# Kernel tuning notes

Hardware: AMD Instinct MI355X
Metric: run time of the kernel (lower is better)

## Reference

```python
import jax, jax.numpy as jnp
import numpy as np
import math

B, L = 16, 4096
N = B * L            # total nodes; node 0 is the (masked) root
E = N - 1            # one parent edge per non-root node
D_IN, D_OUT, HEADS = 512, 256, 4
SLOPE = 0.2          # PyG GATConv default negative_slope
PRUNE_FRAC = 0.3


def gelu(x):
    return 0.5 * x * (1.0 + jnp.tanh(math.sqrt(2.0 / math.pi) * (x + 0.044715 * x ** 3)))


def remove_nodes_func(parent, remove):
    # parent[i] = parent node id of node i+1; remove[j] = 1 iff node j+1 removed.
    for _ in range(5):
        aug_rem = jnp.concatenate([jnp.zeros(1, jnp.int32), remove])
        aug_par = jnp.concatenate([jnp.zeros(1, jnp.int32), parent])
        pr = aug_rem[parent]                               # is my parent removed?
        parent = pr * aug_par[parent] + (1 - pr) * parent  # grandparent if so
    return parent


def remove_nodes_and_edges(edge_index, map_index):
    src, par = edge_index[0], edge_index[1]
    rem = jnp.zeros(N, jnp.int32).at[map_index].set(1)     # removal flag per node id (>=1)
    edge_mask = 1 - rem[src]                               # drop edges whose child node removed
    emr = rem[1:]                                          # == zeros(E).at[map_index-1].set(1)
    temp = remove_nodes_func(par, emr)
    ei_new = jnp.stack([src, temp]) * edge_mask[None, :]   # removed edges collapse to (0,0)
    node_mask_upd = jnp.concatenate([jnp.ones(1, jnp.float32), 1.0 - emr.astype(jnp.float32)])
    return ei_new, node_mask_upd


def gat_conv(xin, edge_index, gat_w, att_src, att_dst, gat_b):
    # PyG GATConv: concat=True, add_self_loops=True, eval mode (attention dropout off)
    h = (xin @ gat_w).reshape(N, HEADS, D_OUT)
    loop = jnp.arange(N, dtype=edge_index.dtype)
    src = jnp.concatenate([edge_index[0], loop])
    dst = jnp.concatenate([edge_index[1], loop])
    a_src = jnp.einsum('nhc,hc->nh', h, att_src)
    a_dst = jnp.einsum('nhc,hc->nh', h, att_dst)
    alpha = jax.nn.leaky_relu(a_src[src] + a_dst[dst], SLOPE)       # [Etot, H]
    m = jax.ops.segment_max(alpha, dst, num_segments=N)
    e = jnp.exp(alpha - m[dst])
    s = jax.ops.segment_sum(e, dst, num_segments=N)
    coef = e / (s[dst] + 1e-16)
    out = jax.ops.segment_sum(coef[:, :, None] * h[src], dst, num_segments=N)
    return out.reshape(N, HEADS * D_OUT) + gat_b


def setup_inputs():
    key = jax.random.key(0)
    ks = jax.random.split(key, 10)
    x = jax.random.normal(ks[0], (N, D_IN), jnp.float32)
    statement_rep = jax.random.normal(ks[1], (N, D_IN), jnp.float32)
    node_mask = (jax.random.uniform(ks[2], (B, L)) > 0.3).astype(jnp.float32)
    node_mask = node_mask.at[0, 0].set(0.0)  # root node never scored/pruned
    type_id = jax.random.randint(ks[3], (B, L), 0, 2, dtype=jnp.int32)
    child = jnp.arange(1, N, dtype=jnp.int32)
    parent = jnp.floor(jax.random.uniform(ks[4], (E,)) * child).astype(jnp.int32)  # parent < child
    edge_index = jnp.stack([child, parent])
    edge_index_ent = edge_index
    s = 0.02
    scorer_w = jax.random.normal(ks[5], (2 * D_IN, 1), jnp.float32) * s
    scorer_b = jnp.zeros((1,), jnp.float32)
    emb_w = jax.random.normal(ks[6], (2, D_OUT), jnp.float32) * s
    emb_b = jnp.zeros((D_OUT,), jnp.float32)
    gat_w = jax.random.normal(ks[7], (2 * D_IN + D_OUT, HEADS * D_OUT), jnp.float32) * s
    att_src = jax.random.normal(ks[8], (HEADS, D_OUT), jnp.float32) * s
    att_dst = jax.random.normal(ks[9], (HEADS, D_OUT), jnp.float32) * s
    gat_b = jnp.zeros((HEADS * D_OUT,), jnp.float32)
    return {"x": x, "edge_index": edge_index, "edge_index_ent": edge_index_ent,
            "statement_rep": statement_rep, "node_mask": node_mask, "type_id": type_id,
            "scorer_w": scorer_w, "scorer_b": scorer_b, "emb_w": emb_w, "emb_b": emb_b,
            "gat_w": gat_w, "att_src": att_src, "att_dst": att_dst, "gat_b": gat_b}


def reference(x, edge_index, edge_index_ent, statement_rep, node_mask, type_id,
              scorer_w, scorer_b, emb_w, emb_b, gat_w, att_src, att_dst, gat_b):
    del edge_index_ent  # threaded through the original but never used
    nm = node_mask.reshape(-1)
    tid = type_id.reshape(-1)
    one_hot = jax.nn.one_hot(tid, 2, dtype=jnp.float32)
    type_emb = gelu(one_hot @ emb_w + emb_b)
    # --- single GNN layer (num_layers=1), with top-k node pruning ---
    node_score = (jnp.concatenate([x, statement_rep], 1) @ scorer_w + scorer_b)[:, 0] * nm
    nnz = int(jnp.count_nonzero(node_score))  # eager; k is data-dependent in the original
    if int(nnz * PRUNE_FRAC) != 0:
        k = int(nnz * PRUNE_FRAC + 1)
        masked = jnp.where(node_score != 0, node_score, jnp.inf)
        _, map_index = jax.lax.top_k(-masked, k)  # k smallest nonzero scores -> node ids
        edge_index, upd = remove_nodes_and_edges(edge_index, map_index)
        nm = nm * upd
    xin = jnp.concatenate([x, statement_rep, type_emb], 1)
    out = gelu(gat_conv(xin, edge_index, gat_w, att_src, att_dst, gat_b))
    # feature dropout runs in eval as identity here (deterministic reference)
    return out, nm.reshape(B, L)
```

## Files before the change

### kernel.cpp

```cpp
#include <hip/hip_runtime.h>
#include <cstdint>
#include <cstddef>

#define N_NODES 65536
#define E_EDGES 65535
#define DIN     512
#define KDIM    1024
#define JDIM    1024
#define HEADS   4
#define DOUT    256

typedef short   short8  __attribute__((ext_vector_type(8)));
typedef float   floatx4 __attribute__((ext_vector_type(4)));

__device__ inline float bf2f(unsigned short u){
  union { unsigned int i; float f; } c; c.i = ((unsigned int)u) << 16; return c.f;
}
__device__ inline unsigned short f2bf(float f){
  union { float f; unsigned int i; } c; c.f = f;
  unsigned int r = c.i + 0x7FFFu + ((c.i >> 16) & 1u);
  return (unsigned short)(r >> 16);
}
__device__ inline unsigned int okey(float f){
  union { float f; unsigned int u; } c; c.f = f;
  return (c.u & 0x80000000u) ? ~c.u : (c.u | 0x80000000u);
}
__device__ inline float unokey(unsigned int k){
  union { unsigned int u; float f; } c;
  c.u = (k & 0x80000000u) ? (k ^ 0x80000000u) : ~k;
  return c.f;
}
__device__ inline float leaky(float x){ return x >= 0.f ? x : 0.2f * x; }
__device__ inline float gelu_f(float x){
  return 0.5f * x * (1.f + tanhf(0.7978845608028654f * (x + 0.044715f * x * x * x)));
}

__global__ void k_prep(const float* __restrict__ x, const float* __restrict__ sr,
                       const float* __restrict__ nmask, const float* __restrict__ sw,
                       const float* __restrict__ sb, unsigned short* __restrict__ xs,
                       float* __restrict__ score){
  int i = blockIdx.x, t = threadIdx.x;
  float4 v;
  if (t < 128) v = *(const float4*)(x  + (size_t)i*DIN + 4*t);
  else         v = *(const float4*)(sr + (size_t)i*DIN + 4*(t-128));
  const float4 w = *(const float4*)(sw + 4*t);
  double part = (double)v.x*(double)w.x + (double)v.y*(double)w.y
              + (double)v.z*(double)w.z + (double)v.w*(double)w.w;
  ushort4 o; o.x = f2bf(v.x); o.y = f2bf(v.y); o.z = f2bf(v.z); o.w = f2bf(v.w);
  *(ushort4*)(xs + (size_t)i*KDIM + 4*t) = o;
  for (int sdel = 32; sdel; sdel >>= 1) part += __shfl_down(part, sdel);
  __shared__ double red[4];
  if ((t & 63) == 0) red[t >> 6] = part;
  __syncthreads();
  if (t == 0){
    double s = red[0] + red[1] + red[2] + red[3] + (double)sb[0];
    score[i] = (float)s * nmask[i];
  }
}

__global__ void k_nnz(const float* __restrict__ score, int* scal){
  int i = blockIdx.x*256 + threadIdx.x;
  int nz = (score[i] != 0.f) ? 1 : 0;
  unsigned long long b = __ballot(nz);
  if ((threadIdx.x & 63) == 0) atomicAdd(&scal[0], (int)__popcll(b));
}

__global__ void k_makekey(const float* __restrict__ score, unsigned int* __restrict__ key){
  int i = blockIdx.x*256 + threadIdx.x;
  float v = score[i];
  if (v == 0.f) v = __builtin_inff();
  key[i] = okey(v);
}

__global__ void k_initsel(int* scal){
  int nnz = scal[0];
  double prod = (double)nnz * 0.3;
  scal[1] = ((int)prod != 0) ? 1 : 0;
  int k = (int)(prod + 1.0);
  scal[2] = k; scal[3] = 0; scal[4] = k;
}

__global__ void k_hist(const unsigned int* __restrict__ key, unsigned int* __restrict__ hist,
                       const int* __restrict__ scal, int pass){
  __shared__ unsigned int lh[256];
  int t = threadIdx.x;
  lh[t] = 0; __syncthreads();
  int i = blockIdx.x*256 + t;
  unsigned int kv = key[i];
  unsigned int pref = (unsigned int)scal[3];
  bool ok = (pass == 0) || ((kv >> (32 - 8*pass)) == pref);
  if (ok) atomicAdd(&lh[(kv >> (24 - 8*pass)) & 255u], 1u);
  __syncthreads();
  if (lh[t]) atomicAdd(&hist[t], lh[t]);
}

__global__ void k_select(unsigned int* __restrict__ hist, int* __restrict__ scal){
  __shared__ unsigned int h[256];
  int t = threadIdx.x;
  h[t] = hist[t];
  __syncthreads();
  if (t == 0){
    unsigned int r = (unsigned int)scal[4];
    unsigned int cum = 0, pref = (unsigned int)scal[3];
    for (int b = 0; b < 256; b++){
      unsigned int c = h[b];
      if (cum + c >= r){
        scal[3] = (int)((pref << 8) | (unsigned int)b);
        scal[4] = (int)(r - cum);
        break;
      }
      cum += c;
    }
  }
  __syncthreads();
  hist[t] = 0;
}

__global__ void k_mark(const unsigned int* __restrict__ key, int* __restrict__ scal,
                       int* __restrict__ rem, int* __restrict__ eqlist){
  if (!scal[1]) return;
  int i = blockIdx.x*256 + threadIdx.x;
  unsigned int Ks = (unsigned int)scal[3];
  unsigned int kv = key[i];
  if (kv < Ks) rem[i] = 1;
  else if (kv == Ks){
    int p = atomicAdd(&scal[5], 1);
    if (p < 4096) eqlist[p] = i;
  }
}

__global__ void k_ties(int* __restrict__ scal, int* __restrict__ eqlist, int* __restrict__ rem){
  if (!scal[1]) return;
  int m = scal[5]; if (m > 4096) m = 4096;
  int need = scal[4]; if (need > m) need = m;
  for (int it = 0; it < need; it++){
    int best = 0x7FFFFFFF, bj = -1;
    for (int j = 0; j < m; j++){ int v = eqlist[j]; if (v < best){ best = v; bj = j; } }
    if (bj < 0) break;
    rem[best] = 1; eqlist[bj] = 0x7FFFFFFF;
  }
}

__global__ void k_remap(const int* __restrict__ pin, const int* __restrict__ rem,
                        int* __restrict__ pout){
  int e = blockIdx.x*256 + threadIdx.x;
  if (e >= E_EDGES) return;
  int p = pin[e];
  pout[e] = rem[p] ? (p == 0 ? 0 : pin[p-1]) : p;
}

__global__ void k_edges(const int* __restrict__ srcIn, const int* __restrict__ pfin,
                        const int* __restrict__ rem, int* __restrict__ srcF,
                        int* __restrict__ dstF, int* __restrict__ cnt){
  int e = blockIdx.x*256 + threadIdx.x;
  if (e >= E_EDGES) return;
  int s = srcIn[e];
  if (rem[s]){ srcF[e] = 0; dstF[e] = -1; }
  else {
    srcF[e] = s;
    int d = pfin[e];
    dstF[e] = d;
    atomicAdd(&cnt[d], 1);
  }
}

__global__ void k_scan1(const int* __restrict__ cnt, int* __restrict__ offs,
                        int* __restrict__ bsum){
  int b = blockIdx.x, t = threadIdx.x, i = b*256 + t;
  int v = cnt[i];
  int lane = t & 63, wv = t >> 6;
  int xv = v;
  for (int o2 = 1; o2 < 64; o2 <<= 1){ int y = __shfl_up(xv, o2); if (lane >= o2) xv += y; }
  __shared__ int wt_[4];
  if (lane == 63) wt_[wv] = xv;
  __syncthreads();
  int add = 0;
  for (int k2 = 0; k2 < wv; k2++) add += wt_[k2];
  offs[i] = xv + add - v;
  if (t == 255) bsum[b] = xv + add;
}

__global__ void k_scan2(int* __restrict__ bsum){
  int t = threadIdx.x;
  int v = bsum[t];
  int lane = t & 63, wv = t >> 6;
  int xv = v;
  for (int o2 = 1; o2 < 64; o2 <<= 1){ int y = __shfl_up(xv, o2); if (lane >= o2) xv += y; }
  __shared__ int wt_[4];
  if (lane == 63) wt_[wv] = xv;
  __syncthreads();
  int add = 0;
  for (int k2 = 0; k2 < wv; k2++) add += wt_[k2];
  bsum[t] = xv + add - v;
}

__global__ void k_scan3(int* __restrict__ offs, const int* __restrict__ bsum,
                        int* __restrict__ cur){
  int b = blockIdx.x, t = threadIdx.x, i = b*256 + t;
  int v = offs[i] + bsum[b];
  offs[i] = v; cur[i] = v;
}

__global__ void k_fill(const int* __restrict__ dstF, int* __restrict__ cur,
                       int* __restrict__ elist){
  int e = blockIdx.x*256 + threadIdx.x;
  if (e >= E_EDGES) return;
  int d = dstF[e]; if (d < 0) return;
  int pos = atomicAdd(&cur[d], 1);
  elist[pos] = e;
}

__global__ void k_wt(const float* __restrict__ gw, unsigned short* __restrict__ wtb){
  __shared__ float tile[32][33];
  int kt = blockIdx.x*32, jt = blockIdx.y*32;
  int tx = threadIdx.x, ty = threadIdx.y;
  for (int r = ty; r < 32; r += 8) tile[r][tx] = gw[(size_t)(kt+r)*JDIM + jt + tx];
  __syncthreads();
  for (int r = ty; r < 32; r += 8) wtb[(size_t)(jt+r)*KDIM + kt + tx] = f2bf(tile[tx][r]);
}

__global__ void k_tc(const float* __restrict__ embw, const float* __restrict__ embb,
                     const float* __restrict__ gw, float* __restrict__ tc){
  int g = blockIdx.x*256 + threadIdx.x;
  int te = g >> 10, j = g & 1023;
  float acc = 0.f;
  for (int c = 0; c < DOUT; c++){
    float e = gelu_f(embw[te*DOUT + c] + embb[c]);
    acc += e * gw[(size_t)(KDIM + c)*JDIM + j];
  }
  tc[te*JDIM + j] = acc;
}

__global__ __launch_bounds__(256) void k_gemm(const unsigned short* __restrict__ xs,
    const unsigned short* __restrict__ wtb, const float* __restrict__ tc,
    const int* __restrict__ tid, unsigned short* __restrict__ hmat){
  __shared__ unsigned short As[128*32];
  __shared__ unsigned short Bs[128*32];
  int bid = blockIdx.x;
  int r8 = bid & 7, tq = bid >> 3;
  int jb = tq & 7, ip = tq >> 3;
  int im = ip*8 + r8;
  int rowbase = im*128, colbase = jb*128;
  int t = threadIdx.x, wave = t >> 6, lane = t & 63;
  int wm = (wave >> 1)*64, wn = (wave & 1)*64;
  floatx4 acc[4][4];
  floatx4 zero = {0.f, 0.f, 0.f, 0.f};
  for (int a = 0; a < 4; a++) for (int b = 0; b < 4; b++) acc[a][b] = zero;
  int lrow = lane >> 2, lkc = (lane & 3)*8;
  for (int kt = 0; kt < 32; kt++){
    int k0 = kt*32;
    for (int hh = 0; hh < 2; hh++){
      int row = hh*64 + wave*16 + lrow;
      const unsigned short* ga = xs  + (size_t)(rowbase + row)*KDIM + k0 + lkc;
      __builtin_amdgcn_global_load_lds((const __attribute__((address_space(1))) void*)ga,
          (__attribute__((address_space(3))) void*)(&As[row*32 + lkc]), 16, 0, 0);
      const unsigned short* gb = wtb + (size_t)(colbase + row)*KDIM + k0 + lkc;
      __builtin_amdgcn_global_load_lds((const __attribute__((address_space(1))) void*)gb,
          (__attribute__((address_space(3))) void*)(&Bs[row*32 + lkc]), 16, 0, 0);
    }
    __syncthreads();
    short8 af[4], bfr[4];
    int rq = (lane >> 4)*8, rr = lane & 15;
    for (int mi = 0; mi < 4; mi++) af[mi]  = *(const short8*)(&As[(wm + mi*16 + rr)*32 + rq]);
    for (int ni = 0; ni < 4; ni++) bfr[ni] = *(const short8*)(&Bs[(wn + ni*16 + rr)*32 + rq]);
    for (int mi = 0; mi < 4; mi++)
      for (int ni = 0; ni < 4; ni++)
        acc[mi][ni] = __builtin_amdgcn_mfma_f32_16x16x32_bf16(af[mi], bfr[ni], acc[mi][ni], 0, 0, 0);
    __syncthreads();
  }
  int q = lane >> 4, cc = lane & 15;
  for (int mi = 0; mi < 4; mi++){
    for (int reg = 0; reg < 4; reg++){
      int rowg = rowbase + wm + mi*16 + q*4 + reg;
      int tt = tid[rowg];
      for (int ni = 0; ni < 4; ni++){
        int col = colbase + wn + ni*16 + cc;
        float v = acc[mi][ni][reg] + tc[tt*JDIM + col];
        hmat[(size_t)rowg*JDIM + col] = f2bf(v);
      }
    }
  }
}

__global__ void k_att(const unsigned short* __restrict__ hmat, const float* __restrict__ atts,
                      const float* __restrict__ attd, float* __restrict__ asrc,
                      float* __restrict__ adst){
  int i = blockIdx.x, t = threadIdx.x;
  int hd = t >> 6, c = (t & 63)*4;
  ushort4 hv = *(const ushort4*)(hmat + (size_t)i*JDIM + hd*DOUT + c);
  float h0 = bf2f(hv.x), h1 = bf2f(hv.y), h2 = bf2f(hv.z), h3 = bf2f(hv.w);
  float4 ws_ = *(const float4*)(atts + hd*DOUT + c);
  float4 wd_ = *(const float4*)(attd + hd*DOUT + c);
  float ps = h0*ws_.x + h1*ws_.y + h2*ws_.z + h3*ws_.w;
  float pd = h0*wd_.x + h1*wd_.y + h2*wd_.z + h3*wd_.w;
  for (int sdel = 32; sdel; sdel >>= 1){ ps += __shfl_down(ps, sdel); pd += __shfl_down(pd, sdel); }
  if ((t & 63) == 0){ asrc[i*HEADS + hd] = ps; adst[i*HEADS + hd] = pd; }
}

__global__ void k_max(const int* __restrict__ srcF, const int* __restrict__ dstF,
                      const float* __restrict__ asrc, const float* __restrict__ adst,
                      unsigned int* __restrict__ mkey){
  int idx = blockIdx.x*256 + threadIdx.x;
  if (idx >= E_EDGES + N_NODES) return;
  int s, d;
  if (idx < E_EDGES){ d = dstF[idx]; if (d < 0) return; s = srcF[idx]; }
  else { s = d = idx - E_EDGES; }
  for (int hd = 0; hd < HEADS; hd++){
    float al = leaky(asrc[s*HEADS + hd] + adst[d*HEADS + hd]);
    atomicMax(&mkey[d*HEADS + hd], okey(al));
  }
}

__global__ void k_sum(const int* __restrict__ srcF, const int* __restrict__ dstF,
                      const float* __restrict__ asrc, const float* __restrict__ adst,
                      const unsigned int* __restrict__ mkey, float* __restrict__ ssum,
                      const int* __restrict__ scal){
  int idx = blockIdx.x*256 + threadIdx.x;
  if (idx >= E_EDGES + N_NODES) return;
  int s, d; float wgt = 1.f;
  if (idx < E_EDGES){ d = dstF[idx]; if (d < 0) return; s = srcF[idx]; }
  else {
    s = d = idx - E_EDGES;
    if (d == 0 && scal[1]) wgt = 1.f + (float)scal[2];
  }
  for (int hd = 0; hd < HEADS; hd++){
    float al = leaky(asrc[s*HEADS + hd] + adst[d*HEADS + hd]);
    float e = expf(al - unokey(mkey[d*HEADS + hd]));
    atomicAdd(&ssum[d*HEADS + hd], wgt * e);
  }
}

__global__ void k_agg(const unsigned short* __restrict__ hmat, const int* __restrict__ srcF,
                      const float* __restrict__ asrc, const float* __restrict__ adst,
                      const unsigned int* __restrict__ mkey, const float* __restrict__ ssum,
                      const int* __restrict__ offs, const int* __restrict__ cnt,
                      const int* __restrict__ elist, const float* __restrict__ gatb,
                      const int* __restrict__ scal, float* __restrict__ out){
  int n = blockIdx.x, t = threadIdx.x;
  int hd = t >> 6;
  float mh = unokey(mkey[n*HEADS + hd]);
  float sh = ssum[n*HEADS + hd] + 1e-16f;
  float adn = adst[n*HEADS + hd];
  float a0 = 0.f, a1 = 0.f, a2 = 0.f, a3 = 0.f;
  {
    float al = leaky(asrc[n*HEADS + hd] + adn);
    float coef = expf(al - mh) / sh;
    if (n == 0 && scal[1]) coef *= (1.f + (float)scal[2]);
    ushort4 hv = *(const ushort4*)(hmat + (size_t)n*JDIM + 4*t);
    a0 += coef*bf2f(hv.x); a1 += coef*bf2f(hv.y); a2 += coef*bf2f(hv.z); a3 += coef*bf2f(hv.w);
  }
  int o0 = offs[n], c_ = cnt[n];
  for (int q2 = 0; q2 < c_; q2++){
    int e = elist[o0 + q2];
    int s = srcF[e];
    float al = leaky(asrc[s*HEADS + hd] + adn);
    float coef = expf(al - mh) / sh;
    ushort4 hv = *(const ushort4*)(hmat + (size_t)s*JDIM + 4*t);
    a0 += coef*bf2f(hv.x); a1 += coef*bf2f(hv.y); a2 += coef*bf2f(hv.z); a3 += coef*bf2f(hv.w);
  }
  const float4 gb = *(const float4*)(gatb + 4*t);
  float4 ov;
  ov.x = gelu_f(a0 + gb.x); ov.y = gelu_f(a1 + gb.y);
  ov.z = gelu_f(a2 + gb.z); ov.w = gelu_f(a3 + gb.w);
  *(float4*)(out + (size_t)n*JDIM + 4*t) = ov;
}

__global__ void k_nm(const float* __restrict__ nmask, const int* __restrict__ rem,
                     float* __restrict__ nmout){
  int i = blockIdx.x*256 + threadIdx.x;
  float u = (i == 0) ? 1.f : (1.f - (float)rem[i]);
  nmout[i] = nmask[i] * u;
}

extern "C" void kernel_launch(void* const* d_in, const int* in_sizes, int n_in,
                              void* d_out, int out_size, void* d_ws, size_t ws_size,
                              hipStream_t stream){
  (void)in_sizes; (void)n_in; (void)out_size; (void)ws_size;
  const float* x    = (const float*)d_in[0];
  const int*  eidx  = (const int*)d_in[1];
  const float* sr   = (const float*)d_in[3];
  const float* nmask= (const float*)d_in[4];
  const int*  tid   = (const int*)d_in[5];
  const float* sw   = (const float*)d_in[6];
  const float* sb   = (const float*)d_in[7];
  const float* embw = (const float*)d_in[8];
  const float* embb = (const float*)d_in[9];
  const float* gw   = (const float*)d_in[10];
  const float* atts = (const float*)d_in[11];
  const float* attd = (const float*)d_in[12];
  const float* gatb = (const float*)d_in[13];
  float* out = (float*)d_out;

  char* w = (char*)d_ws;
  size_t o = 0;
  auto alloc = [&](size_t bytes){ size_t r = o; o += (bytes + 255) & ~(size_t)255; return r; };
  size_t o_cnt  = alloc((size_t)N_NODES*4);
  size_t o_mkey = alloc((size_t)N_NODES*HEADS*4);
  size_t o_ssum = alloc((size_t)N_NODES*HEADS*4);
  size_t o_rem  = alloc((size_t)N_NODES*4);
  size_t o_hist = alloc(256*4);
  size_t o_scal = alloc(64);
  size_t o_eq   = alloc(4096*4);
  size_t zero_bytes = o;
  size_t o_score= alloc((size_t)N_NODES*4);
  size_t o_key  = alloc((size_t)N_NODES*4);
  size_t o_pA   = alloc((size_t)E_EDGES*4);
  size_t o_pB   = alloc((size_t)E_EDGES*4);
  size_t o_srcF = alloc((size_t)E_EDGES*4);
  size_t o_dstF = alloc((size_t)E_EDGES*4);
  size_t o_off  = alloc((size_t)N_NODES*4);
  size_t o_cur  = alloc((size_t)N_NODES*4);
  size_t o_el   = alloc((size_t)E_EDGES*4);
  size_t o_bsum = alloc(256*4);
  size_t o_asrc = alloc((size_t)N_NODES*HEADS*4);
  size_t o_adst = alloc((size_t)N_NODES*HEADS*4);
  size_t o_tc   = alloc((size_t)2*JDIM*4);
  size_t o_wt   = alloc((size_t)JDIM*KDIM*2);
  size_t o_xs   = alloc((size_t)N_NODES*KDIM*2);
  size_t o_h    = alloc((size_t)N_NODES*JDIM*2);

  int* cnt   = (int*)(w + o_cnt);
  unsigned int* mkey = (unsigned int*)(w + o_mkey);
  float* ssum = (float*)(w + o_ssum);
  int* rem   = (int*)(w + o_rem);
  unsigned int* hist = (unsigned int*)(w + o_hist);
  int* scal  = (int*)(w + o_scal);
  int* eqlist= (int*)(w + o_eq);
  float* score = (float*)(w + o_score);
  unsigned int* key = (unsigned int*)(w + o_key);
  int* pA = (int*)(w + o_pA);
  int* pB = (int*)(w + o_pB);
  int* srcF = (int*)(w + o_srcF);
  int* dstF = (int*)(w + o_dstF);
  int* offs = (int*)(w + o_off);
  int* cur  = (int*)(w + o_cur);
  int* elist= (int*)(w + o_el);
  int* bsum = (int*)(w + o_bsum);
  float* asrc = (float*)(w + o_asrc);
  float* adst = (float*)(w + o_adst);
  float* tc = (float*)(w + o_tc);
  unsigned short* wtb = (unsigned short*)(w + o_wt);
  unsigned short* xs  = (unsigned short*)(w + o_xs);
  unsigned short* hmat= (unsigned short*)(w + o_h);

  hipMemsetAsync(w, 0, zero_bytes, stream);

  k_prep<<<N_NODES, 256, 0, stream>>>(x, sr, nmask, sw, sb, xs, score);
  k_nnz<<<N_NODES/256, 256, 0, stream>>>(score, scal);
  k_makekey<<<N_NODES/256, 256, 0, stream>>>(score, key);
  k_initsel<<<1, 1, 0, stream>>>(scal);
  for (int p = 0; p < 4; p++){
    k_hist<<<N_NODES/256, 256, 0, stream>>>(key, hist, scal, p);
    k_select<<<1, 256, 0, stream>>>(hist, scal);
  }
  k_mark<<<N_NODES/256, 256, 0, stream>>>(key, scal, rem, eqlist);
  k_ties<<<1, 1, 0, stream>>>(scal, eqlist, rem);

  const int* par_in = eidx + E_EDGES;
  int egrid = (E_EDGES + 255)/256;
  k_remap<<<egrid, 256, 0, stream>>>(par_in, rem, pA);
  k_remap<<<egrid, 256, 0, stream>>>(pA, rem, pB);
  k_remap<<<egrid, 256, 0, stream>>>(pB, rem, pA);
  k_remap<<<egrid, 256, 0, stream>>>(pA, rem, pB);
  k_remap<<<egrid, 256, 0, stream>>>(pB, rem, pA);

  k_edges<<<egrid, 256, 0, stream>>>(eidx, pA, rem, srcF, dstF, cnt);
  k_scan1<<<256, 256, 0, stream>>>(cnt, offs, bsum);
  k_scan2<<<1, 256, 0, stream>>>(bsum);
  k_scan3<<<256, 256, 0, stream>>>(offs, bsum, cur);
  k_fill<<<egrid, 256, 0, stream>>>(dstF, cur, elist);

  k_wt<<<dim3(32,32), dim3(32,8), 0, stream>>>(gw, wtb);
  k_tc<<<8, 256, 0, stream>>>(embw, embb, gw, tc);
  k_gemm<<<4096, 256, 0, stream>>>(xs, wtb, tc, tid, hmat);
  k_att<<<N_NODES, 256, 0, stream>>>(hmat, atts, attd, asrc, adst);

  int mg = (E_EDGES + N_NODES + 255)/256;
  k_max<<<mg, 256, 0, stream>>>(srcF, dstF, asrc, adst, mkey);
  k_sum<<<mg, 256, 0, stream>>>(srcF, dstF, asrc, adst, mkey, ssum, scal);
  k_agg<<<N_NODES, 256, 0, stream>>>(hmat, srcF, asrc, adst, mkey, ssum, offs, cnt,
                                     elist, gatb, scal, out);
  k_nm<<<N_NODES/256, 256, 0, stream>>>(nmask, rem, out + (size_t)N_NODES*JDIM);
}
```

Before: 1.085 ms.

## Enlarge GEMM tiles to 256x256 with BK=64 and double-buffered LDS staging

The bf16 MFMA projection GEMM moves from 128x128x32 tiles with 4 waves to 256x256x64 tiles with 8 waves. Each wave now computes a 128x64 sub-tile. LDS is double-buffered so the async global-to-LDS loads for the next K step are issued before computing the current one. The goal is higher operand reuse per byte loaded and loads hidden behind MFMA work. In exchange it uses about 128KB of LDS per block, which limits occupancy, carries a large accumulator register footprint, and may cause LDS bank conflicts with the 128-byte unswizzled row stride.

```diff
diff --git a/kernel.cpp b/kernel.cpp
--- a/kernel.cpp
+++ b/kernel.cpp
@@ -231,48 +231,82 @@
   tc[te*JDIM + j] = acc;
 }
 
-__global__ __launch_bounds__(256) void k_gemm(const unsigned short* __restrict__ xs,
+#define BKG 64
+__global__ __launch_bounds__(512, 2) void k_gemm(const unsigned short* __restrict__ xs,
     const unsigned short* __restrict__ wtb, const float* __restrict__ tc,
     const int* __restrict__ tid, unsigned short* __restrict__ hmat){
-  __shared__ unsigned short As[128*32];
-  __shared__ unsigned short Bs[128*32];
+  __shared__ unsigned short As[2][256*BKG];
+  __shared__ unsigned short Bs[2][256*BKG];
   int bid = blockIdx.x;
-  int r8 = bid & 7, tq = bid >> 3;
-  int jb = tq & 7, ip = tq >> 3;
-  int im = ip*8 + r8;
-  int rowbase = im*128, colbase = jb*128;
+  int xcd = bid & 7, tq = bid >> 3;
+  int jb = tq & 3, ip = (tq >> 2)*8 + xcd;
+  int rowbase = ip*256, colbase = jb*256;
   int t = threadIdx.x, wave = t >> 6, lane = t & 63;
-  int wm = (wave >> 1)*64, wn = (wave & 1)*64;
-  floatx4 acc[4][4];
+  int wm = (wave >> 2)*128, wn = (wave & 3)*64;
+  floatx4 acc[8][4];
   floatx4 zero = {0.f, 0.f, 0.f, 0.f};
-  for (int a = 0; a < 4; a++) for (int b = 0; b < 4; b++) acc[a][b] = zero;
-  int lrow = lane >> 2, lkc = (lane & 3)*8;
-  for (int kt = 0; kt < 32; kt++){
-    int k0 = kt*32;
-    for (int hh = 0; hh < 2; hh++){
-      int row = hh*64 + wave*16 + lrow;
-      const unsigned short* ga = xs  + (size_t)(rowbase + row)*KDIM + k0 + lkc;
+  #pragma unroll
+  for (int a = 0; a < 8; a++)
+    #pragma unroll
+    for (int b = 0; b < 4; b++) acc[a][b] = zero;
+
+  int srow = lane >> 3;
+  int scol = (lane & 7)*8;
+
+  auto STAGE = [&](int buf, int kt){
+    int k0 = kt*BKG;
+    #pragma unroll
+    for (int r = 0; r < 4; r++){
+      int ci = r*8 + wave;
+      int row = ci*8 + srow;
+      const unsigned short* ga = xs  + (size_t)(rowbase + row)*KDIM + k0 + scol;
       __builtin_amdgcn_global_load_lds((const __attribute__((address_space(1))) void*)ga,
-          (__attribute__((address_space(3))) void*)(&As[row*32 + lkc]), 16, 0, 0);
-      const unsigned short* gb = wtb + (size_t)(colbase + row)*KDIM + k0 + lkc;
+          (__attribute__((address_space(3))) void*)(&As[buf][ci*512 + lane*8]), 16, 0, 0);
+      const unsigned short* gb = wtb + (size_t)(colbase + row)*KDIM + k0 + scol;
       __builtin_amdgcn_global_load_lds((const __attribute__((address_space(1))) void*)gb,
-          (__attribute__((address_space(3))) void*)(&Bs[row*32 + lkc]), 16, 0, 0);
+          (__attribute__((address_space(3))) void*)(&Bs[buf][ci*512 + lane*8]), 16, 0, 0);
     }
+  };
+
+  int rr = lane & 15, rq = (lane >> 4)*8;
+  auto COMPUTE = [&](int buf){
+    #pragma unroll
+    for (int ks = 0; ks < 2; ks++){
+      short8 af[8], bfr[4];
+      #pragma unroll
+      for (int mi = 0; mi < 8; mi++)
+        af[mi]  = *(const short8*)(&As[buf][(wm + mi*16 + rr)*BKG + ks*32 + rq]);
+      #pragma unroll
+      for (int ni = 0; ni < 4; ni++)
+        bfr[ni] = *(const short8*)(&Bs[buf][(wn + ni*16 + rr)*BKG + ks*32 + rq]);
+      #pragma unroll
+      for (int mi = 0; mi < 8; mi++)
+        #pragma unroll
+        for (int ni = 0; ni < 4; ni++)
+          acc[mi][ni] = __builtin_amdgcn_mfma_f32_16x16x32_bf16(af[mi], bfr[ni], acc[mi][ni], 0, 0, 0);
+    }
+  };
+
+  const int NT = KDIM / BKG;
+  STAGE(0, 0);
+  __syncthreads();
+  int cur = 0;
+  for (int kt = 0; kt < NT - 1; kt++){
+    STAGE(cur ^ 1, kt + 1);
+    COMPUTE(cur);
     __syncthreads();
-    short8 af[4], bfr[4];
-    int rq = (lane >> 4)*8, rr = lane & 15;
-    for (int mi = 0; mi < 4; mi++) af[mi]  = *(const short8*)(&As[(wm + mi*16 + rr)*32 + rq]);
-    for (int ni = 0; ni < 4; ni++) bfr[ni] = *(const short8*)(&Bs[(wn + ni*16 + rr)*32 + rq]);
-    for (int mi = 0; mi < 4; mi++)
-      for (int ni = 0; ni < 4; ni++)
-        acc[mi][ni] = __builtin_amdgcn_mfma_f32_16x16x32_bf16(af[mi], bfr[ni], acc[mi][ni], 0, 0, 0);
-    __syncthreads();
-  }
+    cur ^= 1;
+  }
+  COMPUTE(cur);
+
   int q = lane >> 4, cc = lane & 15;
-  for (int mi = 0; mi < 4; mi++){
+  #pragma unroll
+  for (int mi = 0; mi < 8; mi++){
+    #pragma unroll
     for (int reg = 0; reg < 4; reg++){
       int rowg = rowbase + wm + mi*16 + q*4 + reg;
       int tt = tid[rowg];
+      #pragma unroll
       for (int ni = 0; ni < 4; ni++){
         int col = colbase + wn + ni*16 + cc;
         float v = acc[mi][ni][reg] + tc[tt*JDIM + col];
@@ -472,7 +506,7 @@
 
   k_wt<<<dim3(32,32), dim3(32,8), 0, stream>>>(gw, wtb);
   k_tc<<<8, 256, 0, stream>>>(embw, embb, gw, tc);
-  k_gemm<<<4096, 256, 0, stream>>>(xs, wtb, tc, tid, hmat);
+  k_gemm<<<1024, 512, 0, stream>>>(xs, wtb, tc, tid, hmat);
   k_att<<<N_NODES, 256, 0, stream>>>(hmat, atts, attd, asrc, adst);
 
   int mg = (E_EDGES + N_NODES + 255)/256;
```

After: 1.067 ms. About the same (-1.7%).
